# Kernel optimization log

Hardware: AMD Instinct MI355X
Metric: run time of the kernel (lower is better)

Reference implementation:

```python
import jax, jax.numpy as jnp
import numpy as np

N_NODES = 100000
D_GRAPH = 512    # graph_embedding_dim
D_ROUTE = 1024   # routes_embedding_dim
N_ROUTES = 16384
ROUTE_LEN = 32
N_BLOCKS = 3


def setup_inputs() -> dict:
    key = jax.random.key(0)
    ks = jax.random.split(key, 2 + 2 * N_BLOCKS)
    graph_embedding = jax.random.normal(ks[0], (N_NODES, D_GRAPH), dtype=jnp.float32)
    locations_idx = jax.random.randint(ks[1], (N_ROUTES, ROUTE_LEN), 0, N_NODES, dtype=jnp.int64)
    # Linear block chain: first block D_GRAPH->D_ROUTE, rest D_ROUTE->D_ROUTE, ReLU each
    dims = [D_GRAPH] + [D_ROUTE] * N_BLOCKS
    inp = {"graph_embedding": graph_embedding, "locations_idx": locations_idx}
    for i in range(N_BLOCKS):
        fan_in = dims[i]
        scale = 1.0 / np.sqrt(fan_in)
        inp[f"W{i}"] = jax.random.uniform(ks[2 + 2 * i], (fan_in, dims[i + 1]), jnp.float32, -scale, scale)
        inp[f"b{i}"] = jax.random.uniform(ks[3 + 2 * i], (dims[i + 1],), jnp.float32, -scale, scale)
    return inp


def reference(graph_embedding, locations_idx, W0, b0, W1, b1, W2, b2):
    # per-route gather: [R, L, D] then max over route positions -> [R, D]
    gathered = graph_embedding[locations_idx]          # [n_routes, route_len, d_graph]
    routes_emb = jnp.max(gathered, axis=1)             # [n_routes, d_graph]
    # linear block chain (Linear + ReLU per block)
    x = jax.nn.relu(routes_emb @ W0 + b0)
    x = jax.nn.relu(x @ W1 + b1)
    x = jax.nn.relu(x @ W2 + b2)
    return x
```

## Files before the change

kernel.cpp:

```cpp
#include <hip/hip_runtime.h>
#include <hip/hip_bf16.h>
#include <cstdint>


typedef __attribute__((ext_vector_type(8))) short          bf16x8;
typedef __attribute__((ext_vector_type(8))) unsigned short u16x8;
typedef __attribute__((ext_vector_type(4))) float          f32x4;

__device__ __forceinline__ unsigned short f2b_rne(float f) {
    union { float f; uint32_t i; } x; x.f = f;
    uint32_t lsb = (x.i >> 16) & 1u;
    return (unsigned short)((x.i + 0x7fffu + lsb) >> 16);
}
__device__ __forceinline__ float b2f(unsigned short u) {
    union { float f; uint32_t i; } x; x.i = ((uint32_t)u) << 16; return x.f;
}

__device__ __forceinline__ void async_copy16(const void* gptr, void* lptr) {
    __builtin_amdgcn_global_load_lds(
        (const __attribute__((address_space(1))) unsigned int*)gptr,
        (__attribute__((address_space(3))) unsigned int*)lptr, 16, 0, 0);
}

__global__ __launch_bounds__(256)
void convert_f32_bf16(const float* __restrict__ in, unsigned short* __restrict__ out)
{
    const size_t i = ((size_t)blockIdx.x * 256 + threadIdx.x) * 8;
    const float4* p = reinterpret_cast<const float4*>(in + i);
    float4 v0 = p[0], v1 = p[1];
    u16x8 o;
    o[0] = f2b_rne(v0.x); o[1] = f2b_rne(v0.y); o[2] = f2b_rne(v0.z); o[3] = f2b_rne(v0.w);
    o[4] = f2b_rne(v1.x); o[5] = f2b_rne(v1.y); o[6] = f2b_rne(v1.z); o[7] = f2b_rne(v1.w);
    *reinterpret_cast<u16x8*>(out + i) = o;
}

__global__ void transpose_f32_bf16(const float* __restrict__ W,
                                   unsigned short* __restrict__ Wt,
                                   int K, int N)
{
    __shared__ float tile[32][33];
    const int n0 = blockIdx.x * 32;
    const int k0 = blockIdx.y * 32;
    const int tx = threadIdx.x & 31;
    const int ty = threadIdx.x >> 5;
#pragma unroll
    for (int i = 0; i < 32; i += 8)
        tile[ty + i][tx] = W[(size_t)(k0 + ty + i) * N + (n0 + tx)];
    __syncthreads();
#pragma unroll
    for (int i = 0; i < 32; i += 8)
        Wt[(size_t)(n0 + ty + i) * K + (k0 + tx)] = f2b_rne(tile[tx][ty + i]);
}

__global__ void gather_max_bf16(const unsigned short* __restrict__ graphb,
                                const int* __restrict__ idx32,
                                unsigned short* __restrict__ routes)
{
    bool is64 = true;
#pragma unroll
    for (int k = 0; k < 64; k++) is64 &= (idx32[2 * k + 1] == 0);
    const int stride = is64 ? 64 : 32;
    const int step   = is64 ? 2  : 1;

    const int wave  = threadIdx.x >> 6;
    const int lane  = threadIdx.x & 63;
    const int route = (blockIdx.x * 4 + wave) * 4;
    const int col   = lane * 8;

    float m[4][8];
#pragma unroll
    for (int t = 0; t < 4; t++)
#pragma unroll
        for (int j = 0; j < 8; j++) m[t][j] = -INFINITY;

    const int* ip = idx32 + (size_t)route * stride;
#pragma unroll 2
    for (int l = 0; l < 32; l++) {
        u16x8 v[4];
#pragma unroll
        for (int t = 0; t < 4; t++) {
            const int node = ip[t * stride + l * step];
            v[t] = *reinterpret_cast<const u16x8*>(graphb + (size_t)node * 512 + col);
        }
#pragma unroll
        for (int t = 0; t < 4; t++)
#pragma unroll
            for (int j = 0; j < 8; j++)
                m[t][j] = fmaxf(m[t][j], b2f(v[t][j]));
    }
#pragma unroll
    for (int t = 0; t < 4; t++) {
        u16x8 o;
#pragma unroll
        for (int j = 0; j < 8; j++) {
            union { float f; uint32_t i; } x; x.f = m[t][j];
            o[j] = (unsigned short)(x.i >> 16);
        }
        *reinterpret_cast<u16x8*>(routes + (size_t)(route + t) * 512 + col) = o;
    }
}

__global__ void gather_max_f32(const float* __restrict__ graph,
                               const int* __restrict__ idx32,
                               unsigned short* __restrict__ routes)
{
    bool is64 = true;
#pragma unroll
    for (int k = 0; k < 64; k++) is64 &= (idx32[2 * k + 1] == 0);
    const int stride = is64 ? 64 : 32;
    const int step   = is64 ? 2  : 1;

    const int wave  = threadIdx.x >> 6;
    const int lane  = threadIdx.x & 63;
    const int route = (blockIdx.x * 4 + wave) * 2;
    const int col   = lane * 8;

    float m0[8], m1[8];
#pragma unroll
    for (int j = 0; j < 8; j++) { m0[j] = -INFINITY; m1[j] = -INFINITY; }

    const int* ip0 = idx32 + (size_t)route * stride;
    const int* ip1 = ip0 + stride;
#pragma unroll 4
    for (int l = 0; l < 32; l++) {
        const int n0 = ip0[l * step];
        const int n1 = ip1[l * step];
        const float4* p0 = reinterpret_cast<const float4*>(graph + (size_t)n0 * 512 + col);
        const float4* p1 = reinterpret_cast<const float4*>(graph + (size_t)n1 * 512 + col);
        float4 a0 = p0[0], a1 = p0[1];
        float4 b0 = p1[0], b1 = p1[1];
        m0[0] = fmaxf(m0[0], a0.x); m0[1] = fmaxf(m0[1], a0.y);
        m0[2] = fmaxf(m0[2], a0.z); m0[3] = fmaxf(m0[3], a0.w);
        m0[4] = fmaxf(m0[4], a1.x); m0[5] = fmaxf(m0[5], a1.y);
        m0[6] = fmaxf(m0[6], a1.z); m0[7] = fmaxf(m0[7], a1.w);
        m1[0] = fmaxf(m1[0], b0.x); m1[1] = fmaxf(m1[1], b0.y);
        m1[2] = fmaxf(m1[2], b0.z); m1[3] = fmaxf(m1[3], b0.w);
        m1[4] = fmaxf(m1[4], b1.x); m1[5] = fmaxf(m1[5], b1.y);
        m1[6] = fmaxf(m1[6], b1.z); m1[7] = fmaxf(m1[7], b1.w);
    }
    u16x8 o0, o1;
#pragma unroll
    for (int j = 0; j < 8; j++) { o0[j] = f2b_rne(m0[j]); o1[j] = f2b_rne(m1[j]); }
    *reinterpret_cast<u16x8*>(routes + (size_t)route * 512 + col)       = o0;
    *reinterpret_cast<u16x8*>(routes + (size_t)(route + 1) * 512 + col) = o1;
}

template <int K, typename OutT>
__global__ __launch_bounds__(256)
void gemm_bt_relu(const unsigned short* __restrict__ A,
                  const unsigned short* __restrict__ Bt,
                  const float* __restrict__ bias,
                  OutT* __restrict__ C)
{
    constexpr int N  = 1024;
    constexpr int BK = 64;
    __shared__ unsigned short As[128 * BK];
    __shared__ unsigned short Bs[128 * BK];

    const int tid  = threadIdx.x;
    const int wave = tid >> 6;
    const int lane = tid & 63;
    const int quad = lane >> 4;
    const int l16  = lane & 15;
    const int wm   = (wave >> 1) * 64;
    const int wn   = (wave & 1) * 64;

    const int bm = blockIdx.y * 128;
    const int bn = blockIdx.x * 128;

    int sr[4], sc[4];
    const unsigned short *ag[4], *bg[4];
    unsigned short *al[4], *bl[4];
#pragma unroll
    for (int j = 0; j < 4; j++) {
        const int s = wave * 64 + lane + j * 256;
        const int r = s >> 3;
        const int c = (s & 7) ^ (r & 7);
        sr[j] = r; sc[j] = c;
        ag[j] = A  + (size_t)(bm + r) * K + c * 8;
        bg[j] = Bt + (size_t)(bn + r) * K + c * 8;
        al[j] = As + s * 8;
        bl[j] = Bs + s * 8;
    }

    f32x4 acc[4][4] = {};

    for (int k0 = 0; k0 < K; k0 += BK) {
#pragma unroll
        for (int j = 0; j < 4; j++) async_copy16(ag[j] + k0, al[j]);
#pragma unroll
        for (int j = 0; j < 4; j++) async_copy16(bg[j] + k0, bl[j]);
        __syncthreads();

#pragma unroll
        for (int kk = 0; kk < 2; kk++) {
            const int ch = kk * 4 + quad;
            bf16x8 a[4], b[4];
#pragma unroll
            for (int i = 0; i < 4; i++) {
                const int row = wm + i * 16 + l16;
                a[i] = *reinterpret_cast<const bf16x8*>(
                    As + row * BK + (ch ^ (row & 7)) * 8);
            }
#pragma unroll
            for (int i = 0; i < 4; i++) {
                const int row = wn + i * 16 + l16;
                b[i] = *reinterpret_cast<const bf16x8*>(
                    Bs + row * BK + (ch ^ (row & 7)) * 8);
            }
#pragma unroll
            for (int mi = 0; mi < 4; mi++)
#pragma unroll
                for (int ni = 0; ni < 4; ni++)
                    acc[mi][ni] = __builtin_amdgcn_mfma_f32_16x16x32_bf16(
                        a[mi], b[ni], acc[mi][ni], 0, 0, 0);
        }
        __syncthreads();
    }

#pragma unroll
    for (int ni = 0; ni < 4; ni++) {
        const int n  = bn + wn + ni * 16 + l16;
        const float bv = bias[n];
#pragma unroll
        for (int mi = 0; mi < 4; mi++) {
            const int mbase = bm + wm + mi * 16 + quad * 4;
#pragma unroll
            for (int r = 0; r < 4; r++) {
                float v = acc[mi][ni][r] + bv;
                v = fmaxf(v, 0.0f);
                if constexpr (sizeof(OutT) == 2)
                    C[(size_t)(mbase + r) * N + n] = (OutT)f2b_rne(v);
                else
                    C[(size_t)(mbase + r) * N + n] = (OutT)v;
            }
        }
    }
}

extern "C" void kernel_launch(void* const* d_in, const int* in_sizes, int n_in,
                              void* d_out, int out_size, void* d_ws, size_t ws_size,
                              hipStream_t stream)
{
    constexpr int N_ROUTES = 16384;
    constexpr int N_NODES  = 100000;
    constexpr int D_GRAPH  = 512;
    constexpr int D_ROUTE  = 1024;

    const float* graph = (const float*)d_in[0];
    const int*   idx   = (const int*)d_in[1];
    const float* W0    = (const float*)d_in[2];
    const float* b0    = (const float*)d_in[3];
    const float* W1    = (const float*)d_in[4];
    const float* b1    = (const float*)d_in[5];
    const float* W2    = (const float*)d_in[6];
    const float* b2    = (const float*)d_in[7];
    float*       out   = (float*)d_out;

    char* w = (char*)d_ws;
    unsigned short* Wt0    = (unsigned short*)w; w += (size_t)D_ROUTE * D_GRAPH * 2;
    unsigned short* Wt1    = (unsigned short*)w; w += (size_t)D_ROUTE * D_ROUTE * 2;
    unsigned short* Wt2    = (unsigned short*)w; w += (size_t)D_ROUTE * D_ROUTE * 2;
    unsigned short* routes = (unsigned short*)w; w += (size_t)N_ROUTES * D_GRAPH * 2;
    unsigned short* x1     = (unsigned short*)w; w += (size_t)N_ROUTES * D_ROUTE * 2;
    unsigned short* x2     = (unsigned short*)w; w += (size_t)N_ROUTES * D_ROUTE * 2;
    unsigned short* graphb = (unsigned short*)w;
    const size_t need_bf16 = (size_t)(w - (char*)d_ws) + (size_t)N_NODES * D_GRAPH * 2;
    const bool   use_bf16  = (ws_size >= need_bf16);

    transpose_f32_bf16<<<dim3(D_ROUTE / 32, D_GRAPH / 32), 256, 0, stream>>>(W0, Wt0, D_GRAPH, D_ROUTE);
    transpose_f32_bf16<<<dim3(D_ROUTE / 32, D_ROUTE / 32), 256, 0, stream>>>(W1, Wt1, D_ROUTE, D_ROUTE);
    transpose_f32_bf16<<<dim3(D_ROUTE / 32, D_ROUTE / 32), 256, 0, stream>>>(W2, Wt2, D_ROUTE, D_ROUTE);

    if (use_bf16) {
        convert_f32_bf16<<<(N_NODES * D_GRAPH / 8) / 256, 256, 0, stream>>>(graph, graphb);
        gather_max_bf16<<<N_ROUTES / 16, 256, 0, stream>>>(graphb, idx, routes);
    } else {
        gather_max_f32<<<N_ROUTES / 8, 256, 0, stream>>>(graph, idx, routes);
    }

    gemm_bt_relu<512,  unsigned short><<<dim3(D_ROUTE / 128, N_ROUTES / 128), 256, 0, stream>>>(
        routes, Wt0, b0, x1);
    gemm_bt_relu<1024, unsigned short><<<dim3(D_ROUTE / 128, N_ROUTES / 128), 256, 0, stream>>>(
        x1, Wt1, b1, x2);
    gemm_bt_relu<1024, float><<<dim3(D_ROUTE / 128, N_ROUTES / 128), 256, 0, stream>>>(
        x2, Wt2, b2, out);
}
```

Before: 543.6 us.

## Rewrite GEMM as 256x256 tile, 8-wave, 4-stage pipelined kernel

Replaces the 128x128 single-buffered GEMM with a 256x256-tile kernel using 8 waves, BK=32 and a 4-buffer LDS ring that prefetches three tiles ahead through async global-to-LDS loads. MFMA work is split into two phases interleaved with LDS reads and prefetch issue, ordered by explicit vmcnt waits, barriers and s_setprio. Blocks are remapped with a swizzle to improve L2 reuse. The kernel now launches only 256 blocks, one wave of work across the GPU, which risks lower occupancy and tail imbalance, and it needs more LDS and registers per block.

New measurement: 528.6 us. 2.8% less time.

```diff
diff --git a/kernel.cpp b/kernel.cpp
--- a/kernel.cpp
+++ b/kernel.cpp
@@ -146,76 +146,116 @@
 }
 
 template <int K, typename OutT>
-__global__ __launch_bounds__(256)
-void gemm_bt_relu(const unsigned short* __restrict__ A,
-                  const unsigned short* __restrict__ Bt,
-                  const float* __restrict__ bias,
-                  OutT* __restrict__ C)
+__global__ __launch_bounds__(512, 2)
+void gemm_bt_relu_8p(const unsigned short* __restrict__ A,
+                     const unsigned short* __restrict__ Bt,
+                     const float* __restrict__ bias,
+                     OutT* __restrict__ C)
 {
     constexpr int N  = 1024;
-    constexpr int BK = 64;
-    __shared__ unsigned short As[128 * BK];
-    __shared__ unsigned short Bs[128 * BK];
+    constexpr int BK = 32;
+    constexpr int NT = K / BK;
+
+    __shared__ __align__(16) unsigned short As[4][256 * BK];
+    __shared__ __align__(16) unsigned short Bs[4][256 * BK];
 
     const int tid  = threadIdx.x;
     const int wave = tid >> 6;
     const int lane = tid & 63;
     const int quad = lane >> 4;
     const int l16  = lane & 15;
-    const int wm   = (wave >> 1) * 64;
-    const int wn   = (wave & 1) * 64;
-
-    const int bm = blockIdx.y * 128;
-    const int bn = blockIdx.x * 128;
-
-    int sr[4], sc[4];
-    const unsigned short *ag[4], *bg[4];
-    unsigned short *al[4], *bl[4];
-#pragma unroll
-    for (int j = 0; j < 4; j++) {
-        const int s = wave * 64 + lane + j * 256;
-        const int r = s >> 3;
-        const int c = (s & 7) ^ (r & 7);
-        sr[j] = r; sc[j] = c;
+    const int wm   = (wave >> 2) * 128;
+    const int wn   = (wave & 3) * 64;
+
+    const int swz = (blockIdx.x & 7) * 32 + (blockIdx.x >> 3);
+    const int bm  = (swz >> 2) * 256;
+    const int bn  = (swz & 3) * 256;
+
+    const unsigned short* ag[2];
+    const unsigned short* bg[2];
+    int ao[2];
+#pragma unroll
+    for (int j = 0; j < 2; j++) {
+        const int s = j * 512 + tid;
+        const int r = s >> 2;
+        const int c = (s & 3) ^ ((r >> 1) & 3);
         ag[j] = A  + (size_t)(bm + r) * K + c * 8;
         bg[j] = Bt + (size_t)(bn + r) * K + c * 8;
-        al[j] = As + s * 8;
-        bl[j] = Bs + s * 8;
-    }
-
-    f32x4 acc[4][4] = {};
-
-    for (int k0 = 0; k0 < K; k0 += BK) {
-#pragma unroll
-        for (int j = 0; j < 4; j++) async_copy16(ag[j] + k0, al[j]);
-#pragma unroll
-        for (int j = 0; j < 4; j++) async_copy16(bg[j] + k0, bl[j]);
-        __syncthreads();
-
-#pragma unroll
-        for (int kk = 0; kk < 2; kk++) {
-            const int ch = kk * 4 + quad;
-            bf16x8 a[4], b[4];
-#pragma unroll
-            for (int i = 0; i < 4; i++) {
-                const int row = wm + i * 16 + l16;
-                a[i] = *reinterpret_cast<const bf16x8*>(
-                    As + row * BK + (ch ^ (row & 7)) * 8);
-            }
-#pragma unroll
-            for (int i = 0; i < 4; i++) {
-                const int row = wn + i * 16 + l16;
-                b[i] = *reinterpret_cast<const bf16x8*>(
-                    Bs + row * BK + (ch ^ (row & 7)) * 8);
-            }
-#pragma unroll
-            for (int mi = 0; mi < 4; mi++)
-#pragma unroll
-                for (int ni = 0; ni < 4; ni++)
-                    acc[mi][ni] = __builtin_amdgcn_mfma_f32_16x16x32_bf16(
-                        a[mi], b[ni], acc[mi][ni], 0, 0, 0);
-        }
-        __syncthreads();
+        ao[j] = s * 8;
+    }
+
+#pragma unroll
+    for (int t = 0; t < 3; t++) {
+#pragma unroll
+        for (int j = 0; j < 2; j++) async_copy16(ag[j] + t * BK, &As[t][ao[j]]);
+#pragma unroll
+        for (int j = 0; j < 2; j++) async_copy16(bg[j] + t * BK, &Bs[t][ao[j]]);
+    }
+    asm volatile("s_waitcnt vmcnt(8)" ::: "memory");
+    __builtin_amdgcn_s_barrier();
+
+    f32x4 acc[8][4] = {};
+
+    for (int t = 0; t < NT; ++t) {
+        const unsigned short* Ab = As[t & 3];
+        const unsigned short* Bb = Bs[t & 3];
+
+        bf16x8 bf[4], a0[4];
+#pragma unroll
+        for (int i = 0; i < 4; i++) {
+            const int row = wn + i * 16 + l16;
+            bf[i] = *reinterpret_cast<const bf16x8*>(
+                Bb + row * BK + ((quad ^ ((row >> 1) & 3)) << 3));
+        }
+#pragma unroll
+        for (int i = 0; i < 4; i++) {
+            const int row = wm + i * 16 + l16;
+            a0[i] = *reinterpret_cast<const bf16x8*>(
+                Ab + row * BK + ((quad ^ ((row >> 1) & 3)) << 3));
+        }
+        if (t + 3 < NT) {
+            const int tb = (t + 3) & 3;
+            const int k0 = (t + 3) * BK;
+#pragma unroll
+            for (int j = 0; j < 2; j++) async_copy16(ag[j] + k0, &As[tb][ao[j]]);
+        }
+        __builtin_amdgcn_s_barrier();
+        __builtin_amdgcn_s_setprio(1);
+#pragma unroll
+        for (int mi = 0; mi < 4; mi++)
+#pragma unroll
+            for (int ni = 0; ni < 4; ni++)
+                acc[mi][ni] = __builtin_amdgcn_mfma_f32_16x16x32_bf16(
+                    a0[mi], bf[ni], acc[mi][ni], 0, 0, 0);
+        __builtin_amdgcn_s_setprio(0);
+        __builtin_amdgcn_s_barrier();
+
+        bf16x8 a1[4];
+#pragma unroll
+        for (int i = 0; i < 4; i++) {
+            const int row = wm + 64 + i * 16 + l16;
+            a1[i] = *reinterpret_cast<const bf16x8*>(
+                Ab + row * BK + ((quad ^ ((row >> 1) & 3)) << 3));
+        }
+        if (t + 3 < NT) {
+            const int tb = (t + 3) & 3;
+            const int k0 = (t + 3) * BK;
+#pragma unroll
+            for (int j = 0; j < 2; j++) async_copy16(bg[j] + k0, &Bs[tb][ao[j]]);
+        }
+        __builtin_amdgcn_s_barrier();
+        __builtin_amdgcn_s_setprio(1);
+#pragma unroll
+        for (int mi = 0; mi < 4; mi++)
+#pragma unroll
+            for (int ni = 0; ni < 4; ni++)
+                acc[mi + 4][ni] = __builtin_amdgcn_mfma_f32_16x16x32_bf16(
+                    a1[mi], bf[ni], acc[mi + 4][ni], 0, 0, 0);
+        __builtin_amdgcn_s_setprio(0);
+        if (t + 3 < NT)      asm volatile("s_waitcnt vmcnt(8)" ::: "memory");
+        else if (t + 2 < NT) asm volatile("s_waitcnt vmcnt(4)" ::: "memory");
+        else                 asm volatile("s_waitcnt vmcnt(0)" ::: "memory");
+        __builtin_amdgcn_s_barrier();
     }
 
 #pragma unroll
@@ -223,12 +263,11 @@
         const int n  = bn + wn + ni * 16 + l16;
         const float bv = bias[n];
 #pragma unroll
-        for (int mi = 0; mi < 4; mi++) {
+        for (int mi = 0; mi < 8; mi++) {
             const int mbase = bm + wm + mi * 16 + quad * 4;
 #pragma unroll
             for (int r = 0; r < 4; r++) {
-                float v = acc[mi][ni][r] + bv;
-                v = fmaxf(v, 0.0f);
+                float v = fmaxf(acc[mi][ni][r] + bv, 0.0f);
                 if constexpr (sizeof(OutT) == 2)
                     C[(size_t)(mbase + r) * N + n] = (OutT)f2b_rne(v);
                 else
@@ -279,10 +318,7 @@
         gather_max_f32<<<N_ROUTES / 8, 256, 0, stream>>>(graph, idx, routes);
     }
 
-    gemm_bt_relu<512,  unsigned short><<<dim3(D_ROUTE / 128, N_ROUTES / 128), 256, 0, stream>>>(
-        routes, Wt0, b0, x1);
-    gemm_bt_relu<1024, unsigned short><<<dim3(D_ROUTE / 128, N_ROUTES / 128), 256, 0, stream>>>(
-        x1, Wt1, b1, x2);
-    gemm_bt_relu<1024, float><<<dim3(D_ROUTE / 128, N_ROUTES / 128), 256, 0, stream>>>(
-        x2, Wt2, b2, out);
-}
+    gemm_bt_relu_8p<512,  unsigned short><<<256, 512, 0, stream>>>(routes, Wt0, b0, x1);
+    gemm_bt_relu_8p<1024, unsigned short><<<256, 512, 0, stream>>>(x1, Wt1, b1, x2);
+    gemm_bt_relu_8p<1024, float><<<256, 512, 0, stream>>>(x2, Wt2, b2, out);
+}
```
